# Kernel tuning notes

Hardware: AMD Instinct MI355X
Metric: run time of the kernel (lower is better)

The kernel has to match this reference:

```python
import jax, jax.numpy as jnp
import numpy as np

H = 128  # hidden_dim

def setup_inputs() -> dict:
    key = jax.random.key(0)
    ks = jax.random.split(key, 8)
    B, S = 32, 512
    return {
        "CNN_output": jax.random.normal(ks[0], (B, 4 * S, H), jnp.float32),
        "gaz_input": jax.random.normal(ks[1], (B, S, 128), jnp.float32),
        "gaz_input_back": jax.random.normal(ks[2], (B, S, 128), jnp.float32),
        "global_matrix": jax.random.normal(ks[3], (B, S, H), jnp.float32),
        "exper_input": jax.random.normal(ks[4], (B, S, H), jnp.float32),
        "W_cat": jax.random.normal(ks[5], (3 * H, 16 * H), jnp.float32) * (1.0 / np.sqrt(3 * H)),
        "b_cat": jnp.zeros((16 * H,), jnp.float32),
        "W_exp": jax.random.normal(ks[6], (H, 12 * H), jnp.float32) * (1.0 / np.sqrt(H)),
        "b_exp": jnp.zeros((12 * H,), jnp.float32),
    }


def _diag_gather(y, B, S, width):
    # y: [B, 4*S, 4*width]; for seq-block j pick columns j*width:(j+1)*width
    y = y.reshape(B, 4, S, 4, width)
    j = jnp.arange(4)
    y = y[:, j, :, j, :]              # [4, B, S, width]
    return jnp.transpose(y, (1, 0, 2, 3)).reshape(B, 4 * S, width)


def reference(CNN_output, gaz_input, gaz_input_back, global_matrix, exper_input,
              W_cat, b_cat, W_exp, b_exp):
    B, S4, _ = CNN_output.shape
    S = S4 // 4
    gaz = jnp.concatenate([gaz_input, gaz_input_back, gaz_input, gaz_input_back], axis=1)
    gm = jnp.tile(global_matrix, (1, 4, 1))
    exp_rep = jnp.tile(exper_input, (1, 4, 1))
    cat_in = jnp.concatenate([CNN_output, gaz, gm], axis=2)      # [B, 4S, 3H]
    cat_gates = _diag_gather(cat_in @ W_cat + b_cat, B, S, 4 * H)  # [B, 4S, 4H]
    exper_gates = _diag_gather(exp_rep @ W_exp + b_exp, B, S, 3 * H)  # [B, 4S, 3H]
    new_state = jnp.tanh(cat_gates[:, :, :H])
    gates = jax.nn.sigmoid(cat_gates[:, :, H:] + exper_gates)
    gates = jax.nn.softmax(gates.reshape(B, S4, 3, H), axis=2)
    state_cat = jnp.stack([new_state, CNN_output, exp_rep], axis=2)  # [B, 4S, 3, H]
    layer_output = jnp.sum(gates * state_cat, axis=2)                # [B, 4S, H]
    return tuple(layer_output[:, i * S:(i + 1) * S] for i in range(4))
```

## Files before the change

kernel.cpp:

```cpp
#include <hip/hip_runtime.h>

typedef unsigned short u16;
typedef unsigned int u32;
typedef short bf16x8 __attribute__((ext_vector_type(8)));
typedef float f32x4 __attribute__((ext_vector_type(4)));

#define HH 128

__device__ __forceinline__ u16 f2bf(float f) {
  u32 u = __float_as_uint(f);
  u += 0x7fffu + ((u >> 16) & 1u);
  return (u16)(u >> 16);
}
__device__ __forceinline__ u32 pack2(float a, float b) {
  return (u32)f2bf(a) | ((u32)f2bf(b) << 16);
}
__device__ __forceinline__ float bf2f(u16 h) {
  return __uint_as_float(((u32)h) << 16);
}

__global__ __launch_bounds__(256) void prep_w(const float* __restrict__ Wcat,
                                              const float* __restrict__ Wexp,
                                              u16* __restrict__ Wc) {
  const int bx = blockIdx.x;
  const int nt = bx & 7;
  const int kc = (bx >> 3) & 15;
  const int q = bx >> 7;
  __shared__ u16 T[32 * 72];

  const int tid = threadIdx.x;
  const int r = tid >> 3;
  const int c8 = (tid & 7) * 8;
  float v[8];
  if (kc < 12) {
    const float* src =
        Wcat + (size_t)(kc * 32 + r) * 2048 + q * 512 + nt * 64 + c8;
    float4 a = *(const float4*)src;
    float4 b = *(const float4*)(src + 4);
    v[0] = a.x; v[1] = a.y; v[2] = a.z; v[3] = a.w;
    v[4] = b.x; v[5] = b.y; v[6] = b.z; v[7] = b.w;
  } else if (nt >= 2) {
    const float* src = Wexp + (size_t)((kc - 12) * 32 + r) * 1536 + q * 384 +
                       nt * 64 + c8 - 128;
    float4 a = *(const float4*)src;
    float4 b = *(const float4*)(src + 4);
    v[0] = a.x; v[1] = a.y; v[2] = a.z; v[3] = a.w;
    v[4] = b.x; v[5] = b.y; v[6] = b.z; v[7] = b.w;
  } else {
#pragma unroll
    for (int j = 0; j < 8; ++j) v[j] = 0.f;
  }
  uint4 pk;
  pk.x = pack2(v[0], v[1]);
  pk.y = pack2(v[2], v[3]);
  pk.z = pack2(v[4], v[5]);
  pk.w = pack2(v[6], v[7]);
  *(uint4*)&T[r * 72 + c8] = pk;
  __syncthreads();

  const int p = tid & 3;
  const int nl = tid >> 2;
  const int lq = p ^ (nl & 3) ^ ((nl >> 2) & 3);
  u16 w[8];
#pragma unroll
  for (int j = 0; j < 8; ++j) w[j] = T[(lq * 8 + j) * 72 + nl];
  uint4 o;
  o.x = (u32)w[0] | ((u32)w[1] << 16);
  o.y = (u32)w[2] | ((u32)w[3] << 16);
  o.z = (u32)w[4] | ((u32)w[5] << 16);
  o.w = (u32)w[6] | ((u32)w[7] << 16);
  const size_t idx = ((size_t)((q * 16 + kc) * 512) + nt * 64 + nl) * 4 + p;
  ((uint4*)Wc)[idx] = o;
}

__global__ __launch_bounds__(512, 4) void fused_gate(
    const float* __restrict__ CNN, const float* __restrict__ gaz,
    const float* __restrict__ gazb, const float* __restrict__ gm,
    const float* __restrict__ exper, const u16* __restrict__ Wc,
    const float* __restrict__ bcat, const float* __restrict__ bexp,
    float* __restrict__ out) {
  __shared__ u16 Abuf[16 * 64 * 32];

  const int tid = threadIdx.x;
  const int lane = tid & 63;
  const int wave = tid >> 6;
  const int bx = blockIdx.x;
  const int tile = bx & 7;
  const int grp = bx >> 3;
  const int b = grp >> 2;
  const int q = grp & 3;
  const int s_base = tile * 64;

  const int sel = wave >> 1;
  const float* src_w =
      (sel == 0) ? CNN + (size_t)(b * 2048 + q * 512 + s_base) * HH
      : (sel == 1) ? (((q & 1) ? gazb : gaz) + (size_t)(b * 512 + s_base) * HH)
      : (sel == 2) ? gm + (size_t)(b * 512 + s_base) * HH
                   : exper + (size_t)(b * 512 + s_base) * HH;
#pragma unroll
  for (int t = 0; t < 8; ++t) {
    const int s = t * 64 + lane;
    const int row = (wave & 1) * 32 + (s >> 4);
    const int oct = s & 15;
    const float* sp = src_w + (size_t)row * HH + oct * 8;
    float4 f0 = *(const float4*)sp;
    float4 f1 = *(const float4*)(sp + 4);
    uint4 pk;
    pk.x = pack2(f0.x, f0.y);
    pk.y = pack2(f0.z, f0.w);
    pk.z = pack2(f1.x, f1.y);
    pk.w = pack2(f1.z, f1.w);
    const int kc = sel * 4 + (oct >> 2);
    const int o = oct & 3;
    const int ph = o ^ ((row & 3) ^ ((row >> 2) & 3)) ^ sel;
    *(uint4*)&Abuf[(kc * 64 + row) * 32 + ph * 8] = pk;
  }
  __syncthreads();

  const int l15 = lane & 15;
  const int quad = lane >> 4;
  const int sl = (l15 & 3) ^ ((l15 >> 2) & 3);
  const int physB = quad ^ sl;

  const u16* wp[4];
#pragma unroll
  for (int gg = 0; gg < 4; ++gg) {
    const int n = gg * 128 + wave * 16 + l15;
    wp[gg] = Wc + (((size_t)(q * 16) * 512 + n) * 4 + physB) * 8;
  }

  f32x4 acc[4][4];
#pragma unroll
  for (int rt = 0; rt < 4; ++rt)
#pragma unroll
    for (int gg = 0; gg < 4; ++gg) acc[rt][gg] = (f32x4)0.f;

  bf16x8 bcur[4], bnxt[4];
#pragma unroll
  for (int gg = 0; gg < 4; ++gg) bcur[gg] = *(const bf16x8*)wp[gg];

#pragma unroll
  for (int kc = 0; kc < 16; ++kc) {
    if (kc < 15) {
#pragma unroll
      for (int gg = 0; gg < 4; ++gg)
        bnxt[gg] = *(const bf16x8*)(wp[gg] + (size_t)(kc + 1) * 16384);
    }
    const int pa = (quad ^ sl ^ (kc >> 2)) * 8;
    bf16x8 af[4];
#pragma unroll
    for (int rt = 0; rt < 4; ++rt)
      af[rt] = *(const bf16x8*)&Abuf[(kc * 64 + rt * 16 + l15) * 32 + pa];
#pragma unroll
    for (int rt = 0; rt < 4; ++rt)
#pragma unroll
      for (int gg = 0; gg < 4; ++gg)
        acc[rt][gg] = __builtin_amdgcn_mfma_f32_16x16x32_bf16(
            af[rt], bcur[gg], acc[rt][gg], 0, 0, 0);
#pragma unroll
    for (int gg = 0; gg < 4; ++gg) bcur[gg] = bnxt[gg];
  }

  const float* bcq = bcat + q * 512;
  const float* beq = bexp + q * 384;
  const size_t outbase = (size_t)((q * 32 + b) * 512 + s_base) * HH;
  const int h = wave * 16 + l15;
  const float bc0 = bcq[h];
  const float bc1 = bcq[128 + h];
  const float bc2 = bcq[256 + h];
  const float bc3 = bcq[384 + h];
  const float be1 = beq[h];
  const float be2 = beq[128 + h];
  const float be3 = beq[256 + h];
  const int kcc = h >> 5;
  const int kce = 12 + (h >> 5);
  const int oh = (h >> 3) & 3;
  const int he = h & 7;
#pragma unroll
  for (int rt = 0; rt < 4; ++rt) {
#pragma unroll
    for (int r = 0; r < 4; ++r) {
      const int row = rt * 16 + quad * 4 + r;
      const int srw = (row & 3) ^ ((row >> 2) & 3);
      const float cnn = bf2f(Abuf[(kcc * 64 + row) * 32 + (oh ^ srw) * 8 + he]);
      const float ex =
          bf2f(Abuf[(kce * 64 + row) * 32 + (oh ^ srw ^ 3) * 8 + he]);
      const float c0 = acc[rt][0][r] + bc0;
      const float p1 = acc[rt][1][r] + bc1 + be1;
      const float p2 = acc[rt][2][r] + bc2 + be2;
      const float p3 = acc[rt][3][r] + bc3 + be3;
      const float e2c = __expf(2.f * c0);
      const float ns = 1.f - 2.f * __builtin_amdgcn_rcpf(e2c + 1.f);
      const float g1 = __builtin_amdgcn_rcpf(1.f + __expf(-p1));
      const float g2 = __builtin_amdgcn_rcpf(1.f + __expf(-p2));
      const float g3 = __builtin_amdgcn_rcpf(1.f + __expf(-p3));
      const float e1 = __expf(g1);
      const float e2 = __expf(g2);
      const float e3 = __expf(g3);
      const float inv = __builtin_amdgcn_rcpf(e1 + e2 + e3);
      out[outbase + (size_t)row * HH + h] = (e1 * ns + e2 * cnn + e3 * ex) * inv;
    }
  }
}

extern "C" void kernel_launch(void* const* d_in, const int* in_sizes, int n_in,
                              void* d_out, int out_size, void* d_ws, size_t ws_size,
                              hipStream_t stream) {
  const float* CNN = (const float*)d_in[0];
  const float* gaz = (const float*)d_in[1];
  const float* gazb = (const float*)d_in[2];
  const float* gm = (const float*)d_in[3];
  const float* exper = (const float*)d_in[4];
  const float* Wcat = (const float*)d_in[5];
  const float* bcat = (const float*)d_in[6];
  const float* Wexp = (const float*)d_in[7];
  const float* bexp = (const float*)d_in[8];
  u16* Wc = (u16*)d_ws;

  prep_w<<<512, 256, 0, stream>>>(Wcat, Wexp, Wc);
  fused_gate<<<1024, 512, 0, stream>>>(CNN, gaz, gazb, gm, exper, Wc, bcat,
                                       bexp, (float*)d_out);
}
```

Before: 155.9 us.

## Stream A-tile loads chunk by chunk, overlapping global loads with MFMA compute

```diff
diff --git a/kernel.cpp b/kernel.cpp
--- a/kernel.cpp
+++ b/kernel.cpp
@@ -91,18 +91,17 @@
   const int q = grp & 3;
   const int s_base = tile * 64;
 
-  const int sel = wave >> 1;
-  const float* src_w =
-      (sel == 0) ? CNN + (size_t)(b * 2048 + q * 512 + s_base) * HH
-      : (sel == 1) ? (((q & 1) ? gazb : gaz) + (size_t)(b * 512 + s_base) * HH)
-      : (sel == 2) ? gm + (size_t)(b * 512 + s_base) * HH
-                   : exper + (size_t)(b * 512 + s_base) * HH;
-#pragma unroll
-  for (int t = 0; t < 8; ++t) {
-    const int s = t * 64 + lane;
-    const int row = (wave & 1) * 32 + (s >> 4);
-    const int oct = s & 15;
-    const float* sp = src_w + (size_t)row * HH + oct * 8;
+  const int arow = tid >> 3;
+  const int ao = tid & 7;
+  const int akcl = ao >> 2;
+  const int aoo = ao & 3;
+  const int asw = (arow & 3) ^ ((arow >> 2) & 3);
+  const int cnnoff = (b * 2048 + q * 512 + s_base + arow) * HH;
+  const int stdoff = (b * 512 + s_base + arow) * HH;
+  const float* gz = (q & 1) ? gazb : gaz;
+
+  {
+    const float* sp = CNN + cnnoff + ao * 8;
     float4 f0 = *(const float4*)sp;
     float4 f1 = *(const float4*)(sp + 4);
     uint4 pk;
@@ -110,10 +109,9 @@
     pk.y = pack2(f0.z, f0.w);
     pk.z = pack2(f1.x, f1.y);
     pk.w = pack2(f1.z, f1.w);
-    const int kc = sel * 4 + (oct >> 2);
-    const int o = oct & 3;
-    const int ph = o ^ ((row & 3) ^ ((row >> 2) & 3)) ^ sel;
-    *(uint4*)&Abuf[(kc * 64 + row) * 32 + ph * 8] = pk;
+    const int kc = akcl;
+    const int ph = aoo ^ asw;
+    *(uint4*)&Abuf[(kc * 64 + arow) * 32 + ph * 8] = pk;
   }
   __syncthreads();
 
@@ -121,13 +119,11 @@
   const int quad = lane >> 4;
   const int sl = (l15 & 3) ^ ((l15 >> 2) & 3);
   const int physB = quad ^ sl;
-
-  const u16* wp[4];
-#pragma unroll
-  for (int gg = 0; gg < 4; ++gg) {
-    const int n = gg * 128 + wave * 16 + l15;
-    wp[gg] = Wc + (((size_t)(q * 16) * 512 + n) * 4 + physB) * 8;
-  }
+  const u16* wq = Wc + q * 262144;
+  int nofs[4];
+#pragma unroll
+  for (int gg = 0; gg < 4; ++gg)
+    nofs[gg] = ((gg * 128 + wave * 16 + l15) * 4 + physB) * 8;
 
   f32x4 acc[4][4];
 #pragma unroll
@@ -137,33 +133,60 @@
 
   bf16x8 bcur[4], bnxt[4];
 #pragma unroll
-  for (int gg = 0; gg < 4; ++gg) bcur[gg] = *(const bf16x8*)wp[gg];
-
-#pragma unroll
-  for (int kc = 0; kc < 16; ++kc) {
-    if (kc < 15) {
-#pragma unroll
-      for (int gg = 0; gg < 4; ++gg)
-        bnxt[gg] = *(const bf16x8*)(wp[gg] + (size_t)(kc + 1) * 16384);
-    }
-    const int pa = (quad ^ sl ^ (kc >> 2)) * 8;
-    bf16x8 af[4];
-#pragma unroll
-    for (int rt = 0; rt < 4; ++rt)
-      af[rt] = *(const bf16x8*)&Abuf[(kc * 64 + rt * 16 + l15) * 32 + pa];
-#pragma unroll
-    for (int rt = 0; rt < 4; ++rt)
-#pragma unroll
-      for (int gg = 0; gg < 4; ++gg)
-        acc[rt][gg] = __builtin_amdgcn_mfma_f32_16x16x32_bf16(
-            af[rt], bcur[gg], acc[rt][gg], 0, 0, 0);
-#pragma unroll
-    for (int gg = 0; gg < 4; ++gg) bcur[gg] = bnxt[gg];
+  for (int gg = 0; gg < 4; ++gg) bcur[gg] = *(const bf16x8*)(wq + nofs[gg]);
+
+#pragma unroll
+  for (int c = 0; c < 8; ++c) {
+    float4 f0, f1;
+    if (c < 7) {
+      const int cc = c + 1;
+      const int sel = cc >> 1;
+      const float* base = (sel == 0) ? CNN + cnnoff
+                          : (sel == 1) ? gz + stdoff
+                          : (sel == 2) ? gm + stdoff
+                                       : exper + stdoff;
+      const float* sp = base + (cc & 1) * 64 + ao * 8;
+      f0 = *(const float4*)sp;
+      f1 = *(const float4*)(sp + 4);
+    }
+#pragma unroll
+    for (int k2 = 0; k2 < 2; ++k2) {
+      const int kc = c * 2 + k2;
+      if (kc < 15) {
+#pragma unroll
+        for (int gg = 0; gg < 4; ++gg)
+          bnxt[gg] = *(const bf16x8*)(wq + (kc + 1) * 16384 + nofs[gg]);
+      }
+      const int pa = (quad ^ sl ^ (kc >> 2)) * 8;
+      bf16x8 af[4];
+#pragma unroll
+      for (int rt = 0; rt < 4; ++rt)
+        af[rt] = *(const bf16x8*)&Abuf[(kc * 64 + rt * 16 + l15) * 32 + pa];
+#pragma unroll
+      for (int rt = 0; rt < 4; ++rt)
+#pragma unroll
+        for (int gg = 0; gg < 4; ++gg)
+          acc[rt][gg] = __builtin_amdgcn_mfma_f32_16x16x32_bf16(
+              af[rt], bcur[gg], acc[rt][gg], 0, 0, 0);
+#pragma unroll
+      for (int gg = 0; gg < 4; ++gg) bcur[gg] = bnxt[gg];
+    }
+    if (c < 7) {
+      uint4 pk;
+      pk.x = pack2(f0.x, f0.y);
+      pk.y = pack2(f0.z, f0.w);
+      pk.z = pack2(f1.x, f1.y);
+      pk.w = pack2(f1.z, f1.w);
+      const int kc = (c + 1) * 2 + akcl;
+      const int ph = aoo ^ asw ^ ((c + 1) >> 1);
+      *(uint4*)&Abuf[(kc * 64 + arow) * 32 + ph * 8] = pk;
+      __syncthreads();
+    }
   }
 
   const float* bcq = bcat + q * 512;
   const float* beq = bexp + q * 384;
-  const size_t outbase = (size_t)((q * 32 + b) * 512 + s_base) * HH;
+  const int outbase = ((q * 32 + b) * 512 + s_base) * HH;
   const int h = wave * 16 + l15;
   const float bc0 = bcq[h];
   const float bc1 = bcq[128 + h];
@@ -198,7 +221,7 @@
       const float e2 = __expf(g2);
       const float e3 = __expf(g3);
       const float inv = __builtin_amdgcn_rcpf(e1 + e2 + e3);
-      out[outbase + (size_t)row * HH + h] = (e1 * ns + e2 * cnn + e3 * ex) * inv;
+      out[outbase + row * HH + h] = (e1 * ns + e2 * cnn + e3 * ex) * inv;
     }
   }
 }
```

Result: slower. 178.5 us (+14.5%).

## Pre-convert activations to bf16 and stage them into LDS via direct DMA

Applied to the files above, without the earlier changes.

```diff
diff --git a/kernel.cpp b/kernel.cpp
--- a/kernel.cpp
+++ b/kernel.cpp
@@ -18,6 +18,18 @@
 __device__ __forceinline__ float bf2f(u16 h) {
   return __uint_as_float(((u32)h) << 16);
 }
+
+__device__ __forceinline__ void lds_dma16(const void* g, void* l) {
+  __builtin_amdgcn_global_load_lds(
+      (const __attribute__((address_space(1))) u32*)g,
+      (__attribute__((address_space(3))) u32*)l, 16, 0, 0);
+}
+
+#define AB_CNN 0
+#define AB_GAZ 8388608
+#define AB_GAZB 10485760
+#define AB_GM 12582912
+#define AB_EXP 14680064
 
 __global__ __launch_bounds__(256) void prep_w(const float* __restrict__ Wcat,
                                               const float* __restrict__ Wexp,
@@ -73,10 +85,40 @@
   ((uint4*)Wc)[idx] = o;
 }
 
-__global__ __launch_bounds__(512, 4) void fused_gate(
+__global__ __launch_bounds__(256) void prep_a(
     const float* __restrict__ CNN, const float* __restrict__ gaz,
     const float* __restrict__ gazb, const float* __restrict__ gm,
-    const float* __restrict__ exper, const u16* __restrict__ Wc,
+    const float* __restrict__ exper, u16* __restrict__ Ab) {
+  const int gid = blockIdx.x * 256 + threadIdx.x;
+  const int i0 = gid * 32;
+  const float* src;
+  int off;
+  if (i0 < AB_GAZ) {
+    src = CNN; off = i0 - AB_CNN;
+  } else if (i0 < AB_GAZB) {
+    src = gaz; off = i0 - AB_GAZ;
+  } else if (i0 < AB_GM) {
+    src = gazb; off = i0 - AB_GAZB;
+  } else if (i0 < AB_EXP) {
+    src = gm; off = i0 - AB_GM;
+  } else {
+    src = exper; off = i0 - AB_EXP;
+  }
+#pragma unroll
+  for (int j = 0; j < 4; ++j) {
+    float4 a = *(const float4*)(src + off + j * 8);
+    float4 b = *(const float4*)(src + off + j * 8 + 4);
+    uint4 pk;
+    pk.x = pack2(a.x, a.y);
+    pk.y = pack2(a.z, a.w);
+    pk.z = pack2(b.x, b.y);
+    pk.w = pack2(b.z, b.w);
+    *(uint4*)(Ab + i0 + j * 8) = pk;
+  }
+}
+
+__global__ __launch_bounds__(512, 4) void fused_gate(
+    const u16* __restrict__ Wc, const u16* __restrict__ Ab,
     const float* __restrict__ bcat, const float* __restrict__ bexp,
     float* __restrict__ out) {
   __shared__ u16 Abuf[16 * 64 * 32];
@@ -91,43 +133,45 @@
   const int q = grp & 3;
   const int s_base = tile * 64;
 
-  const int sel = wave >> 1;
-  const float* src_w =
-      (sel == 0) ? CNN + (size_t)(b * 2048 + q * 512 + s_base) * HH
-      : (sel == 1) ? (((q & 1) ? gazb : gaz) + (size_t)(b * 512 + s_base) * HH)
-      : (sel == 2) ? gm + (size_t)(b * 512 + s_base) * HH
-                   : exper + (size_t)(b * 512 + s_base) * HH;
-#pragma unroll
-  for (int t = 0; t < 8; ++t) {
-    const int s = t * 64 + lane;
-    const int row = (wave & 1) * 32 + (s >> 4);
-    const int oct = s & 15;
-    const float* sp = src_w + (size_t)row * HH + oct * 8;
-    float4 f0 = *(const float4*)sp;
-    float4 f1 = *(const float4*)(sp + 4);
-    uint4 pk;
-    pk.x = pack2(f0.x, f0.y);
-    pk.y = pack2(f0.z, f0.w);
-    pk.z = pack2(f1.x, f1.y);
-    pk.w = pack2(f1.z, f1.w);
-    const int kc = sel * 4 + (oct >> 2);
-    const int o = oct & 3;
-    const int ph = o ^ ((row & 3) ^ ((row >> 2) & 3)) ^ sel;
-    *(uint4*)&Abuf[(kc * 64 + row) * 32 + ph * 8] = pk;
-  }
-  __syncthreads();
+  const int cnn_b = AB_CNN + (b * 2048 + q * 512 + s_base) * HH;
+  const int gaz_b = AB_GAZ + (q & 1) * 2097152 + (b * 512 + s_base) * HH;
+  const int gm_b = AB_GM + (b * 512 + s_base) * HH;
+  const int exp_b = AB_EXP + (b * 512 + s_base) * HH;
+  const int rloc = lane >> 2;
+  const int oph = lane & 3;
+#pragma unroll
+  for (int jj = 0; jj < 2; ++jj) {
+    const int j = wave + jj * 8;
+    const int sel = j >> 2;
+    const int sb = (sel == 0) ? cnn_b
+                 : (sel == 1) ? gaz_b
+                 : (sel == 2) ? gm_b
+                              : exp_b;
+#pragma unroll
+    for (int t = 0; t < 4; ++t) {
+      const int row = t * 16 + rloc;
+      const int o = oph ^ ((row & 3) ^ ((row >> 2) & 3)) ^ sel;
+      lds_dma16(Ab + sb + row * HH + (j & 3) * 32 + o * 8,
+                &Abuf[(j * 64 + t * 16) * 32]);
+    }
+  }
 
   const int l15 = lane & 15;
   const int quad = lane >> 4;
   const int sl = (l15 & 3) ^ ((l15 >> 2) & 3);
   const int physB = quad ^ sl;
-
-  const u16* wp[4];
-#pragma unroll
-  for (int gg = 0; gg < 4; ++gg) {
-    const int n = gg * 128 + wave * 16 + l15;
-    wp[gg] = Wc + (((size_t)(q * 16) * 512 + n) * 4 + physB) * 8;
-  }
+  const u16* wq = Wc + q * 262144;
+  int nofs[4];
+#pragma unroll
+  for (int gg = 0; gg < 4; ++gg)
+    nofs[gg] = ((gg * 128 + wave * 16 + l15) * 4 + physB) * 8;
+
+  bf16x8 b0[4], b1[4];
+#pragma unroll
+  for (int gg = 0; gg < 4; ++gg) b0[gg] = *(const bf16x8*)(wq + nofs[gg]);
+#pragma unroll
+  for (int gg = 0; gg < 4; ++gg)
+    b1[gg] = *(const bf16x8*)(wq + 16384 + nofs[gg]);
 
   f32x4 acc[4][4];
 #pragma unroll
@@ -135,35 +179,30 @@
 #pragma unroll
     for (int gg = 0; gg < 4; ++gg) acc[rt][gg] = (f32x4)0.f;
 
-  bf16x8 bcur[4], bnxt[4];
-#pragma unroll
-  for (int gg = 0; gg < 4; ++gg) bcur[gg] = *(const bf16x8*)wp[gg];
+  __syncthreads();
 
 #pragma unroll
   for (int kc = 0; kc < 16; ++kc) {
-    if (kc < 15) {
-#pragma unroll
-      for (int gg = 0; gg < 4; ++gg)
-        bnxt[gg] = *(const bf16x8*)(wp[gg] + (size_t)(kc + 1) * 16384);
-    }
     const int pa = (quad ^ sl ^ (kc >> 2)) * 8;
     bf16x8 af[4];
 #pragma unroll
     for (int rt = 0; rt < 4; ++rt)
       af[rt] = *(const bf16x8*)&Abuf[(kc * 64 + rt * 16 + l15) * 32 + pa];
 #pragma unroll
-    for (int rt = 0; rt < 4; ++rt)
-#pragma unroll
-      for (int gg = 0; gg < 4; ++gg)
+    for (int gg = 0; gg < 4; ++gg) {
+      bf16x8* bc = (kc & 1) ? b1 : b0;
+#pragma unroll
+      for (int rt = 0; rt < 4; ++rt)
         acc[rt][gg] = __builtin_amdgcn_mfma_f32_16x16x32_bf16(
-            af[rt], bcur[gg], acc[rt][gg], 0, 0, 0);
-#pragma unroll
-    for (int gg = 0; gg < 4; ++gg) bcur[gg] = bnxt[gg];
+            af[rt], bc[gg], acc[rt][gg], 0, 0, 0);
+      if (kc < 14)
+        bc[gg] = *(const bf16x8*)(wq + (kc + 2) * 16384 + nofs[gg]);
+    }
   }
 
   const float* bcq = bcat + q * 512;
   const float* beq = bexp + q * 384;
-  const size_t outbase = (size_t)((q * 32 + b) * 512 + s_base) * HH;
+  const int outbase = ((q * 32 + b) * 512 + s_base) * HH;
   const int h = wave * 16 + l15;
   const float bc0 = bcq[h];
   const float bc1 = bcq[128 + h];
@@ -181,7 +220,7 @@
 #pragma unroll
     for (int r = 0; r < 4; ++r) {
       const int row = rt * 16 + quad * 4 + r;
-      const int srw = (row & 3) ^ ((row >> 2) & 3);
+      const int srw = r ^ quad;
       const float cnn = bf2f(Abuf[(kcc * 64 + row) * 32 + (oh ^ srw) * 8 + he]);
       const float ex =
           bf2f(Abuf[(kce * 64 + row) * 32 + (oh ^ srw ^ 3) * 8 + he]);
@@ -198,7 +237,7 @@
       const float e2 = __expf(g2);
       const float e3 = __expf(g3);
       const float inv = __builtin_amdgcn_rcpf(e1 + e2 + e3);
-      out[outbase + (size_t)row * HH + h] = (e1 * ns + e2 * cnn + e3 * ex) * inv;
+      out[outbase + row * HH + h] = (e1 * ns + e2 * cnn + e3 * ex) * inv;
     }
   }
 }
@@ -216,8 +255,9 @@
   const float* Wexp = (const float*)d_in[7];
   const float* bexp = (const float*)d_in[8];
   u16* Wc = (u16*)d_ws;
+  u16* Ab = Wc + 1048576;
 
   prep_w<<<512, 256, 0, stream>>>(Wcat, Wexp, Wc);
-  fused_gate<<<1024, 512, 0, stream>>>(CNN, gaz, gazb, gm, exper, Wc, bcat,
-                                       bexp, (float*)d_out);
-}
+  prep_a<<<2048, 256, 0, stream>>>(CNN, gaz, gazb, gm, exper, Ab);
+  fused_gate<<<1024, 512, 0, stream>>>(Wc, Ab, bcat, bexp, (float*)d_out);
+}
```

New measurement: 172.5 us. 1.11x slower.
